# Optimization experiments

Hardware: AMD Instinct MI355X
Metric: run time of the kernel (lower is better)

Reference implementation:

```python
import jax, jax.numpy as jnp
import numpy as np

N_NODES = 100000
N_EDGES = 1000000
IN_FEAT = 128
OUT_FEAT = 128
NUM_RELS = 64
NUM_BASES = 16
SUBMAT_IN = IN_FEAT // NUM_BASES   # 8
SUBMAT_OUT = OUT_FEAT // NUM_BASES # 8


def setup_inputs() -> dict:
    key = jax.random.key(0)
    k = jax.random.split(key, 8)
    h = jax.random.normal(k[0], (N_NODES, IN_FEAT), dtype=jnp.float32)
    norm = jax.random.uniform(k[1], (N_EDGES, 1), dtype=jnp.float32)
    src = jax.random.randint(k[2], (N_EDGES,), 0, N_NODES, dtype=jnp.int32)
    dst = jax.random.randint(k[3], (N_EDGES,), 0, N_NODES, dtype=jnp.int32)
    r = jax.random.randint(k[4], (N_EDGES,), 0, NUM_RELS, dtype=jnp.int32)
    # learned params (xavier-uniform style scale)
    wscale = np.sqrt(6.0 / (SUBMAT_IN + SUBMAT_OUT)) * np.sqrt(2.0)
    weight = jax.random.uniform(k[5], (NUM_RELS, NUM_BASES * SUBMAT_IN * SUBMAT_OUT),
                                minval=-wscale, maxval=wscale, dtype=jnp.float32)
    lscale = np.sqrt(6.0 / (IN_FEAT + OUT_FEAT)) * np.sqrt(2.0)
    loop_weight = jax.random.uniform(k[6], (IN_FEAT, OUT_FEAT),
                                     minval=-lscale, maxval=lscale, dtype=jnp.float32)
    h_bias = jnp.zeros((OUT_FEAT,), dtype=jnp.float32)
    return {"h": h, "norm": norm, "weight": weight, "loop_weight": loop_weight,
            "h_bias": h_bias, "src": src, "dst": dst, "r": r}


def reference(h, norm, weight, loop_weight, h_bias, src, dst, r):
    E = src.shape[0]
    # per-edge block-diagonal weights: (E, B, si, so)
    w = weight[r].reshape(E, NUM_BASES, SUBMAT_IN, SUBMAT_OUT)
    # src features split into blocks: (E, B, si)
    hs = h[src].reshape(E, NUM_BASES, SUBMAT_IN)
    # small bmm per block, flatten to (E, OUT_FEAT)
    msg = jnp.einsum('ebi,ebio->ebo', hs, w).reshape(E, OUT_FEAT)
    msg = msg * norm
    # scatter-sum to destination nodes
    agg = jax.ops.segment_sum(msg, dst, num_segments=N_NODES)
    # self-loop message (dropout=0.0) + bias
    out = agg + h_bias + h @ loop_weight
    return jax.nn.relu(out)
```

## Files before the change

kernel.cpp:

```cpp
#include <hip/hip_runtime.h>
#include <stdint.h>

#define N_NODES 100000
#define N_EDGES 1000000
#define IN_F 128
#define OUT_F 128
#define NUM_RELS 64
#define NB_SCAN ((N_NODES + 255) / 256)
#define N_WAVES 16384
#define GATHER_B 256

typedef _Float16 half2v __attribute__((ext_vector_type(2)));

__device__ __forceinline__ float dot2f(uint32_t hu, uint32_t wu, float acc) {
#if __has_builtin(__builtin_amdgcn_fdot2)
    return __builtin_amdgcn_fdot2(__builtin_bit_cast(half2v, hu),
                                  __builtin_bit_cast(half2v, wu), acc, false);
#else
    half2v a = __builtin_bit_cast(half2v, hu);
    half2v b = __builtin_bit_cast(half2v, wu);
    acc = fmaf((float)a.x, (float)b.x, acc);
    acc = fmaf((float)a.y, (float)b.y, acc);
    return acc;
#endif
}

__device__ __forceinline__ uint32_t pkh2(float x, float y) {
    half2v v;
    v.x = (_Float16)x;
    v.y = (_Float16)y;
    return __builtin_bit_cast(uint32_t, v);
}

__global__ __launch_bounds__(256) void gemm_selfloop(
    const float* __restrict__ h, const float* __restrict__ W,
    const float* __restrict__ bias, float* __restrict__ out, int n_nodes)
{
    const int tid = threadIdx.x;
    const int ty = tid >> 4, tx = tid & 15;
    const int node0 = blockIdx.x * 128 + ty * 8;
    const int o0 = tx * 8;

    float acc[8][8];
#pragma unroll
    for (int j = 0; j < 8; ++j)
#pragma unroll
        for (int i = 0; i < 8; ++i) acc[j][i] = 0.f;

    int nidx[8];
#pragma unroll
    for (int j = 0; j < 8; ++j) {
        int n = node0 + j;
        nidx[j] = n < n_nodes ? n : (n_nodes - 1);
    }

    for (int k = 0; k < IN_F; k += 4) {
        float hsv[8][4];
#pragma unroll
        for (int j = 0; j < 8; ++j) {
            float4 hv = *reinterpret_cast<const float4*>(h + (size_t)nidx[j] * IN_F + k);
            *reinterpret_cast<float4*>(hsv[j]) = hv;
        }
#pragma unroll
        for (int kk = 0; kk < 4; ++kk) {
            const float* wrow = W + (size_t)(k + kk) * OUT_F + o0;
            float wr[8];
            *reinterpret_cast<float4*>(wr)     = *reinterpret_cast<const float4*>(wrow);
            *reinterpret_cast<float4*>(wr + 4) = *reinterpret_cast<const float4*>(wrow + 4);
#pragma unroll
            for (int j = 0; j < 8; ++j) {
                const float hk = hsv[j][kk];
#pragma unroll
                for (int i = 0; i < 8; ++i)
                    acc[j][i] = fmaf(hk, wr[i], acc[j][i]);
            }
        }
    }

    float br[8];
    *reinterpret_cast<float4*>(br)     = *reinterpret_cast<const float4*>(bias + o0);
    *reinterpret_cast<float4*>(br + 4) = *reinterpret_cast<const float4*>(bias + o0 + 4);

#pragma unroll
    for (int j = 0; j < 8; ++j) {
        int n = node0 + j;
        if (n < n_nodes) {
            float4 v0, v1;
            v0.x = acc[j][0] + br[0]; v0.y = acc[j][1] + br[1];
            v0.z = acc[j][2] + br[2]; v0.w = acc[j][3] + br[3];
            v1.x = acc[j][4] + br[4]; v1.y = acc[j][5] + br[5];
            v1.z = acc[j][6] + br[6]; v1.w = acc[j][7] + br[7];
            float* op = out + (size_t)n * OUT_F + o0;
            *reinterpret_cast<float4*>(op)     = v0;
            *reinterpret_cast<float4*>(op + 4) = v1;
        }
    }
}

__global__ __launch_bounds__(256) void prep_hist_h16(
    const float* __restrict__ weight, uint32_t* __restrict__ wsw,
    const int* __restrict__ dst, int* __restrict__ cnt,
    const float* __restrict__ h, uint4* __restrict__ h16_4,
    int n_edges, int do_h16)
{
    int t = blockIdx.x * 256 + threadIdx.x;
    if (t < NUM_RELS * 512) {
        int r    = t >> 9;
        int p    = t & 511;
        int half = p >> 8;
        int w8   = p & 255;
        int l    = w8 >> 2;
        int ip   = w8 & 3;
        int b    = l >> 2;
        int q    = l & 3;
        int o    = 2 * q + half;
        const float* s = weight + (size_t)r * 1024 + b * 64 + (2 * ip) * 8 + o;
        half2v v;
        v.x = (_Float16)s[0];
        v.y = (_Float16)s[8];
        wsw[t] = __builtin_bit_cast(uint32_t, v);
        return;
    }
    int e = t - NUM_RELS * 512;
    if (e < n_edges) {
        atomicAdd(&cnt[dst[e]], 1);
        return;
    }
    if (!do_h16) return;
    int t2 = e - n_edges;
    if (t2 < N_NODES * IN_F / 8) {
        const float4* hp = reinterpret_cast<const float4*>(h + (size_t)t2 * 8);
        float4 a = hp[0], c = hp[1];
        uint4 r;
        r.x = pkh2(a.x, a.y);
        r.y = pkh2(a.z, a.w);
        r.z = pkh2(c.x, c.y);
        r.w = pkh2(c.z, c.w);
        h16_4[t2] = r;
    }
}

__global__ __launch_bounds__(256) void block_sums(
    const int* __restrict__ cnt, int* __restrict__ part, int n)
{
    __shared__ int sdata[256];
    int i = blockIdx.x * 256 + threadIdx.x;
    sdata[threadIdx.x] = (i < n) ? cnt[i] : 0;
    __syncthreads();
    for (int s = 128; s > 0; s >>= 1) {
        if (threadIdx.x < s) sdata[threadIdx.x] += sdata[threadIdx.x + s];
        __syncthreads();
    }
    if (threadIdx.x == 0) part[blockIdx.x] = sdata[0];
}

__global__ __launch_bounds__(256) void write_off2(
    const int* __restrict__ cnt, const int* __restrict__ part,
    int* __restrict__ off, int* __restrict__ cur, int n, int n_edges)
{
    __shared__ int sdata[256];
    __shared__ int buf[256];
    const int tid = threadIdx.x;
    const int bid = blockIdx.x;

    int psum = 0;
    for (int t = tid; t < bid; t += 256) psum += part[t];
    sdata[tid] = psum;
    __syncthreads();
    for (int s = 128; s > 0; s >>= 1) {
        if (tid < s) sdata[tid] += sdata[tid + s];
        __syncthreads();
    }
    const int blockoff = sdata[0];

    int i = bid * 256 + tid;
    int v = (i < n) ? cnt[i] : 0;
    buf[tid] = v;
    __syncthreads();
    for (int ofs = 1; ofs < 256; ofs <<= 1) {
        int t = (tid >= ofs) ? buf[tid - ofs] : 0;
        __syncthreads();
        buf[tid] += t;
        __syncthreads();
    }
    int excl = buf[tid] - v + blockoff;
    if (i < n) { off[i] = excl; cur[i] = excl; }
    if (i == n - 1) off[n] = n_edges;
}

__global__ __launch_bounds__(256) void fill_and_part(
    const int* __restrict__ src, const int* __restrict__ dst,
    const int* __restrict__ rel, const float* __restrict__ norm,
    int* __restrict__ cur, int2* __restrict__ emeta,
    const int* __restrict__ off, int* __restrict__ wstart, int n_edges)
{
    int t = blockIdx.x * 256 + threadIdx.x;
    if (t < n_edges) {
        int d = dst[t];
        int p = atomicAdd(&cur[d], 1);
        int2 m;
        m.x = src[t] | (rel[t] << 20);
        m.y = __float_as_int(norm[t]);
        emeta[p] = m;
    } else {
        int w = t - n_edges;
        if (w <= N_WAVES) {
            if (w == 0) {
                wstart[0] = 0;
            } else if (w == N_WAVES) {
                wstart[N_WAVES] = N_NODES;
            } else {
                int target = (int)(((long long)N_EDGES * w) / N_WAVES);
                int lo = 0, hi = N_NODES - 1;
                while (lo < hi) {
                    int mid = (lo + hi) >> 1;
                    if (off[mid + 1] > target) hi = mid; else lo = mid + 1;
                }
                wstart[w] = lo;
            }
        } else if (w <= N_WAVES + 3) {
            int2 z; z.x = 0; z.y = 0;
            emeta[n_edges + (w - N_WAVES - 1)] = z;
        }
    }
}

__global__ __launch_bounds__(1024, 4) void gather_nodes10(
    const uint4* __restrict__ h16_4, const uint32_t* __restrict__ wsw,
    const int* __restrict__ off, const int2* __restrict__ emeta,
    const int* __restrict__ wstart, float* __restrict__ out)
{
    __shared__ uint32_t wlds[NUM_RELS * 512];

    {
        uint4* l4 = reinterpret_cast<uint4*>(wlds);
        const uint4* g4 = reinterpret_cast<const uint4*>(wsw);
        int t = threadIdx.x;
#pragma unroll
        for (int k = 0; k < 8; ++k)
            l4[t + k * 1024] = g4[t + k * 1024];
    }
    __syncthreads();

    const int lane = threadIdx.x & 63;
    const int wid  = threadIdx.x >> 6;
    const int b = lane >> 2;
    const int q = lane & 3;
    const uint32_t lbase = (uint32_t)(lane * 4);

    for (int wv = blockIdx.x * 16 + wid; wv < N_WAVES; wv += GATHER_B * 16) {
        const int n0 = wstart[wv];
        const int n1 = wstart[wv + 1];
        if (n0 >= n1) continue;

        int j = off[n0];
        int e_next = off[n0 + 1];

        int2 m0 = emeta[j];
        int2 m1 = emeta[j + 1];
        int2 m2 = emeta[j + 2];
        uint4 hv0 = h16_4[((uint32_t)m0.x & 0xFFFFFu) * 16 + b];
        uint4 hv1 = h16_4[((uint32_t)m1.x & 0xFFFFFu) * 16 + b];

        uint32_t base0 = ((uint32_t)m0.x >> 20) * 512 + lbase;
        uint4 wa = *reinterpret_cast<const uint4*>(&wlds[base0]);
        uint4 wb = *reinterpret_cast<const uint4*>(&wlds[base0 + 256]);

        for (int d = n0; d < n1; ++d) {
            const int idx2 = (d + 2 < n1) ? d + 2 : n1;
            const int e_nn = off[idx2];
            float a0 = 0.f, a1 = 0.f;

            while (j < e_next) {
                int2 m3 = emeta[j + 3];
                uint4 hv2 = h16_4[((uint32_t)m2.x & 0xFFFFFu) * 16 + b];
                uint32_t bn = ((uint32_t)m1.x >> 20) * 512 + lbase;
                uint4 wna = *reinterpret_cast<const uint4*>(&wlds[bn]);
                uint4 wnb = *reinterpret_cast<const uint4*>(&wlds[bn + 256]);

                float s0 = dot2f(hv0.x, wa.x, 0.f);
                s0 = dot2f(hv0.y, wa.y, s0);
                s0 = dot2f(hv0.z, wa.z, s0);
                s0 = dot2f(hv0.w, wa.w, s0);
                float s1 = dot2f(hv0.x, wb.x, 0.f);
                s1 = dot2f(hv0.y, wb.y, s1);
                s1 = dot2f(hv0.z, wb.z, s1);
                s1 = dot2f(hv0.w, wb.w, s1);

                const float nm = __int_as_float(m0.y);
                a0 = fmaf(s0, nm, a0);
                a1 = fmaf(s1, nm, a1);

                m0 = m1; m1 = m2; m2 = m3;
                hv0 = hv1; hv1 = hv2;
                wa = wna; wb = wnb;
                ++j;
            }

            float2* op = reinterpret_cast<float2*>(out + (size_t)d * OUT_F + b * 8 + 2 * q);
            float2 bse = *op;
            float2 res;
            res.x = fmaxf(bse.x + a0, 0.f);
            res.y = fmaxf(bse.y + a1, 0.f);
            *op = res;

            e_next = e_nn;
        }
    }
}

__global__ __launch_bounds__(1024, 4) void gather_nodes6(
    const float* __restrict__ h, const uint32_t* __restrict__ wsw,
    const int* __restrict__ off, const int2* __restrict__ emeta,
    const int* __restrict__ wstart, float* __restrict__ out)
{
    __shared__ uint32_t wlds[NUM_RELS * 512];
    {
        uint4* l4 = reinterpret_cast<uint4*>(wlds);
        const uint4* g4 = reinterpret_cast<const uint4*>(wsw);
        int t = threadIdx.x;
#pragma unroll
        for (int k = 0; k < 8; ++k)
            l4[t + k * 1024] = g4[t + k * 1024];
    }
    __syncthreads();

    const int lane = threadIdx.x & 63;
    const int wid  = threadIdx.x >> 6;
    const int b = lane >> 2;
    const int q = lane & 3;
    const uint32_t lbase = (uint32_t)(lane * 4);

    for (int wv = blockIdx.x * 16 + wid; wv < N_WAVES; wv += GATHER_B * 16) {
        const int n0 = wstart[wv];
        const int n1 = wstart[wv + 1];
        if (n0 >= n1) continue;

        int j = off[n0];
        int2 m0 = emeta[j];
        int2 m1 = emeta[j + 1];
        int2 m2 = emeta[j + 2];

        const float4* hr0 = reinterpret_cast<const float4*>(
            h + (size_t)((uint32_t)m0.x & 0xFFFFFu) * IN_F + b * 8);
        float4 h0A = hr0[0], h0B = hr0[1];
        const float4* hr1 = reinterpret_cast<const float4*>(
            h + (size_t)((uint32_t)m1.x & 0xFFFFFu) * IN_F + b * 8);
        float4 h1A = hr1[0], h1B = hr1[1];

        uint32_t base0 = ((uint32_t)m0.x >> 20) * 512 + lbase;
        uint4 wa = *reinterpret_cast<const uint4*>(&wlds[base0]);
        uint4 wb = *reinterpret_cast<const uint4*>(&wlds[base0 + 256]);

        for (int d = n0; d < n1; ++d) {
            const int end_d = off[d + 1];
            float a0 = 0.f, a1 = 0.f;

            while (j < end_d) {
                int2 m3 = emeta[j + 3];
                const float4* hr2 = reinterpret_cast<const float4*>(
                    h + (size_t)((uint32_t)m2.x & 0xFFFFFu) * IN_F + b * 8);
                float4 h2A = hr2[0], h2B = hr2[1];
                uint32_t bn = ((uint32_t)m1.x >> 20) * 512 + lbase;
                uint4 wna = *reinterpret_cast<const uint4*>(&wlds[bn]);
                uint4 wnb = *reinterpret_cast<const uint4*>(&wlds[bn + 256]);

                uint32_t h01 = __builtin_bit_cast(uint32_t, __builtin_amdgcn_cvt_pkrtz(h0A.x, h0A.y));
                uint32_t h23 = __builtin_bit_cast(uint32_t, __builtin_amdgcn_cvt_pkrtz(h0A.z, h0A.w));
                uint32_t h45 = __builtin_bit_cast(uint32_t, __builtin_amdgcn_cvt_pkrtz(h0B.x, h0B.y));
                uint32_t h67 = __builtin_bit_cast(uint32_t, __builtin_amdgcn_cvt_pkrtz(h0B.z, h0B.w));

                float s0 = dot2f(h01, wa.x, 0.f);
                s0 = dot2f(h23, wa.y, s0);
                s0 = dot2f(h45, wa.z, s0);
                s0 = dot2f(h67, wa.w, s0);
                float s1 = dot2f(h01, wb.x, 0.f);
                s1 = dot2f(h23, wb.y, s1);
                s1 = dot2f(h45, wb.z, s1);
                s1 = dot2f(h67, wb.w, s1);

                const float nm = __int_as_float(m0.y);
                a0 = fmaf(s0, nm, a0);
                a1 = fmaf(s1, nm, a1);

                m0 = m1; m1 = m2; m2 = m3;
                h0A = h1A; h0B = h1B; h1A = h2A; h1B = h2B;
                wa = wna; wb = wnb;
                ++j;
            }

            float2* op = reinterpret_cast<float2*>(out + (size_t)d * OUT_F + b * 8 + 2 * q);
            float2 bse = *op;
            float2 res;
            res.x = fmaxf(bse.x + a0, 0.f);
            res.y = fmaxf(bse.y + a1, 0.f);
            *op = res;
        }
    }
}

extern "C" void kernel_launch(void* const* d_in, const int* in_sizes, int n_in,
                              void* d_out, int out_size, void* d_ws, size_t ws_size,
                              hipStream_t stream)
{
    const float* h      = (const float*)d_in[0];
    const float* norm   = (const float*)d_in[1];
    const float* weight = (const float*)d_in[2];
    const float* loop_w = (const float*)d_in[3];
    const float* bias   = (const float*)d_in[4];
    const int*   src    = (const int*)d_in[5];
    const int*   dst    = (const int*)d_in[6];
    const int*   rel    = (const int*)d_in[7];
    float* out = (float*)d_out;

    char* wsb = (char*)d_ws;
    char* ws0 = wsb;
    int*  cnt    = (int*)wsb;  wsb += sizeof(int) * N_NODES;
    int*  off    = (int*)wsb;  wsb += sizeof(int) * (N_NODES + 1);
    int*  cur    = (int*)wsb;  wsb += sizeof(int) * N_NODES;
    int*  part   = (int*)wsb;  wsb += sizeof(int) * 512;
    int*  wstart = (int*)wsb;  wsb += sizeof(int) * (N_WAVES + 1);
    wsb = (char*)(((uintptr_t)wsb + 15) & ~(uintptr_t)15);
    uint32_t* wsw = (uint32_t*)wsb; wsb += sizeof(uint32_t) * NUM_RELS * 512;
    int2* emeta = (int2*)wsb;  wsb += sizeof(int2) * (N_EDGES + 3);
    wsb = (char*)(((uintptr_t)wsb + 15) & ~(uintptr_t)15);
    uint4* h16_4 = (uint4*)wsb; wsb += (size_t)N_NODES * IN_F * 2;

    const int use_h16 = (size_t)(wsb - ws0) <= ws_size;

    hipMemsetAsync(cnt, 0, sizeof(int) * N_NODES, stream);

    const int h16_threads = use_h16 ? (N_NODES * IN_F / 8) : 0;
    const int prep_blocks = (NUM_RELS * 512 + N_EDGES + h16_threads + 255) / 256;
    prep_hist_h16<<<prep_blocks, 256, 0, stream>>>(weight, wsw, dst, cnt,
                                                   h, h16_4, N_EDGES, use_h16);
    block_sums<<<NB_SCAN, 256, 0, stream>>>(cnt, part, N_NODES);
    write_off2<<<NB_SCAN, 256, 0, stream>>>(cnt, part, off, cur, N_NODES, N_EDGES);
    const int fp_grid = (N_EDGES + N_WAVES + 4 + 255) / 256;
    fill_and_part<<<fp_grid, 256, 0, stream>>>(src, dst, rel, norm, cur, emeta,
                                               off, wstart, N_EDGES);

    gemm_selfloop<<<(N_NODES + 127) / 128, 256, 0, stream>>>(h, loop_w, bias, out, N_NODES);
    if (use_h16) {
        gather_nodes10<<<GATHER_B, 1024, 0, stream>>>(h16_4, wsw, off, emeta, wstart, out);
    } else {
        gather_nodes6<<<GATHER_B, 1024, 0, stream>>>(h, wsw, off, emeta, wstart, out);
    }
}
```

Baseline: 319.7 us.

## Fuse the whole RGCN pipeline into one cooperative kernel with grid syncs

Replaces the memset plus six separate launches (weight swizzle, histogram, fp16 conversion, scan, CSR fill, self-loop GEMM and gather) with one cooperative persistent kernel of 256 blocks × 1024 threads. The stages are separated by grid.sync() calls, and the scan is redone with wave shuffles. The aim is to remove per-launch overhead and the idle gaps between the small preprocessing kernels. In exchange, the GEMM body now runs under a 1024-thread launch bound and may suffer register pressure. The non-cooperative fallback now always calls the fp16 gather, even when h16 does not fit in the workspace.

```diff
diff --git a/kernel.cpp b/kernel.cpp
--- a/kernel.cpp
+++ b/kernel.cpp
@@ -1,5 +1,8 @@
 #include <hip/hip_runtime.h>
+#include <hip/hip_cooperative_groups.h>
 #include <stdint.h>
+
+namespace cg = cooperative_groups;
 
 #define N_NODES 100000
 #define N_EDGES 1000000
@@ -9,6 +12,8 @@
 #define NB_SCAN ((N_NODES + 255) / 256)
 #define N_WAVES 16384
 #define GATHER_B 256
+#define GEMM_TILES ((N_NODES + 127) / 128)
+#define H16_ITEMS (N_NODES * IN_F / 8)
 
 typedef _Float16 half2v __attribute__((ext_vector_type(2)));
 
@@ -32,13 +37,22 @@
     return __builtin_bit_cast(uint32_t, v);
 }
 
-__global__ __launch_bounds__(256) void gemm_selfloop(
+__device__ __forceinline__ int wave_incl_scan(int v, int lane) {
+#pragma unroll
+    for (int o = 1; o < 64; o <<= 1) {
+        int t = __shfl_up(v, o);
+        if (lane >= o) v += t;
+    }
+    return v;
+}
+
+__device__ __forceinline__ void gemm_tile_body(
     const float* __restrict__ h, const float* __restrict__ W,
-    const float* __restrict__ bias, float* __restrict__ out, int n_nodes)
-{
-    const int tid = threadIdx.x;
+    const float* __restrict__ bias, float* __restrict__ out,
+    int tile, int tid)
+{
     const int ty = tid >> 4, tx = tid & 15;
-    const int node0 = blockIdx.x * 128 + ty * 8;
+    const int node0 = tile * 128 + ty * 8;
     const int o0 = tx * 8;
 
     float acc[8][8];
@@ -51,7 +65,7 @@
 #pragma unroll
     for (int j = 0; j < 8; ++j) {
         int n = node0 + j;
-        nidx[j] = n < n_nodes ? n : (n_nodes - 1);
+        nidx[j] = n < N_NODES ? n : (N_NODES - 1);
     }
 
     for (int k = 0; k < IN_F; k += 4) {
@@ -84,7 +98,7 @@
 #pragma unroll
     for (int j = 0; j < 8; ++j) {
         int n = node0 + j;
-        if (n < n_nodes) {
+        if (n < N_NODES) {
             float4 v0, v1;
             v0.x = acc[j][0] + br[0]; v0.y = acc[j][1] + br[1];
             v0.z = acc[j][2] + br[2]; v0.w = acc[j][3] + br[3];
@@ -97,6 +111,235 @@
     }
 }
 
+__device__ __forceinline__ void wsw_write_one(
+    const float* __restrict__ weight, uint32_t* __restrict__ wsw, int t)
+{
+    int r    = t >> 9;
+    int p    = t & 511;
+    int half = p >> 8;
+    int w8   = p & 255;
+    int l    = w8 >> 2;
+    int ip   = w8 & 3;
+    int b    = l >> 2;
+    int q    = l & 3;
+    int o    = 2 * q + half;
+    const float* s = weight + (size_t)r * 1024 + b * 64 + (2 * ip) * 8 + o;
+    half2v v;
+    v.x = (_Float16)s[0];
+    v.y = (_Float16)s[8];
+    wsw[t] = __builtin_bit_cast(uint32_t, v);
+}
+
+__device__ __forceinline__ void h16_write_one(
+    const float* __restrict__ h, uint4* __restrict__ h16_4, int t2)
+{
+    const float4* hp = reinterpret_cast<const float4*>(h + (size_t)t2 * 8);
+    float4 a = hp[0], c = hp[1];
+    uint4 r;
+    r.x = pkh2(a.x, a.y);
+    r.y = pkh2(a.z, a.w);
+    r.z = pkh2(c.x, c.y);
+    r.w = pkh2(c.z, c.w);
+    h16_4[t2] = r;
+}
+
+__global__ __launch_bounds__(1024, 4) void coop_all(
+    const float* __restrict__ h, const float* __restrict__ norm_,
+    const float* __restrict__ weight, const float* __restrict__ loop_w,
+    const float* __restrict__ bias, const int* __restrict__ src,
+    const int* __restrict__ dst, const int* __restrict__ rel,
+    float* __restrict__ out, int* __restrict__ cnt, int* __restrict__ off,
+    int* __restrict__ cur, int* __restrict__ part, int* __restrict__ wstart,
+    uint32_t* __restrict__ wsw, int2* __restrict__ emeta,
+    uint4* __restrict__ h16_4)
+{
+    __shared__ uint32_t wlds[NUM_RELS * 512];
+    __shared__ int wsum[16];
+
+    cg::grid_group grid = cg::this_grid();
+
+    const int tid  = threadIdx.x;
+    const int gtid = blockIdx.x * 1024 + tid;
+    const int NT   = GATHER_B * 1024;
+    const int lane = tid & 63;
+
+    for (int i = gtid; i < N_NODES; i += NT) cnt[i] = 0;
+    if (gtid < NUM_RELS * 512) wsw_write_one(weight, wsw, gtid);
+    for (int t2 = gtid; t2 < H16_ITEMS; t2 += NT) h16_write_one(h, h16_4, t2);
+    {
+        int group = gtid >> 8;
+        if (group < GEMM_TILES)
+            gemm_tile_body(h, loop_w, bias, out, group, gtid & 255);
+    }
+    grid.sync();
+
+    for (int e = gtid; e < N_EDGES; e += NT)
+        atomicAdd(&cnt[dst[e]], 1);
+    grid.sync();
+
+    {
+        int gw = gtid >> 6;
+        if (gw < NB_SCAN) {
+            int s = 0;
+#pragma unroll
+            for (int k = 0; k < 4; ++k) {
+                int idx = gw * 256 + k * 64 + lane;
+                s += (idx < N_NODES) ? cnt[idx] : 0;
+            }
+#pragma unroll
+            for (int o = 32; o > 0; o >>= 1) s += __shfl_xor(s, o);
+            if (lane == 0) part[gw] = s;
+        }
+    }
+    grid.sync();
+
+    if (blockIdx.x == 0) {
+        const int wid = tid >> 6;
+        if (tid < 512) {
+            int v = (tid < NB_SCAN) ? part[tid] : 0;
+            int incl = wave_incl_scan(v, lane);
+            if (lane == 63) wsum[wid] = incl;
+            __syncthreads();
+            if (wid == 0) {
+                int sv = (lane < 8) ? wsum[lane] : 0;
+                int si = wave_incl_scan(sv, lane);
+                if (lane < 8) wsum[lane] = si - sv;
+            }
+            __syncthreads();
+            part[tid] = incl - v + wsum[wid];
+        } else {
+            __syncthreads();
+            __syncthreads();
+        }
+    }
+    grid.sync();
+
+    {
+        int gw = gtid >> 6;
+        if (gw < NB_SCAN) {
+            int carry = part[gw];
+#pragma unroll
+            for (int k = 0; k < 4; ++k) {
+                int idx = gw * 256 + k * 64 + lane;
+                int v = (idx < N_NODES) ? cnt[idx] : 0;
+                int incl = wave_incl_scan(v, lane);
+                int o = carry + incl - v;
+                if (idx < N_NODES) { off[idx] = o; cur[idx] = o; }
+                carry += __shfl(incl, 63);
+            }
+        }
+        if (gtid == 0) off[N_NODES] = N_EDGES;
+    }
+    grid.sync();
+
+    for (int e = gtid; e < N_EDGES; e += NT) {
+        int d = dst[e];
+        int p = atomicAdd(&cur[d], 1);
+        int2 m;
+        m.x = src[e] | (rel[e] << 20);
+        m.y = __float_as_int(norm_[e]);
+        emeta[p] = m;
+    }
+    for (int w = gtid; w <= N_WAVES; w += NT) {
+        if (w == 0) {
+            wstart[0] = 0;
+        } else if (w == N_WAVES) {
+            wstart[N_WAVES] = N_NODES;
+        } else {
+            int target = (int)(((long long)N_EDGES * w) / N_WAVES);
+            int lo = 0, hi = N_NODES - 1;
+            while (lo < hi) {
+                int mid = (lo + hi) >> 1;
+                if (off[mid + 1] > target) hi = mid; else lo = mid + 1;
+            }
+            wstart[w] = lo;
+        }
+    }
+    if (gtid < 3) { int2 z; z.x = 0; z.y = 0; emeta[N_EDGES + gtid] = z; }
+    grid.sync();
+
+    {
+        uint4* l4 = reinterpret_cast<uint4*>(wlds);
+        const uint4* g4 = reinterpret_cast<const uint4*>(wsw);
+#pragma unroll
+        for (int k = 0; k < 8; ++k)
+            l4[tid + k * 1024] = g4[tid + k * 1024];
+    }
+    __syncthreads();
+
+    const int wid  = tid >> 6;
+    const int b = lane >> 2;
+    const int q = lane & 3;
+    const uint32_t lbase = (uint32_t)(lane * 4);
+
+    for (int wv = blockIdx.x * 16 + wid; wv < N_WAVES; wv += GATHER_B * 16) {
+        const int n0 = wstart[wv];
+        const int n1 = wstart[wv + 1];
+        if (n0 >= n1) continue;
+
+        int j = off[n0];
+        int e_next = off[n0 + 1];
+
+        int2 m0 = emeta[j];
+        int2 m1 = emeta[j + 1];
+        int2 m2 = emeta[j + 2];
+        uint4 hv0 = h16_4[((uint32_t)m0.x & 0xFFFFFu) * 16 + b];
+        uint4 hv1 = h16_4[((uint32_t)m1.x & 0xFFFFFu) * 16 + b];
+
+        uint32_t base0 = ((uint32_t)m0.x >> 20) * 512 + lbase;
+        uint4 wa = *reinterpret_cast<const uint4*>(&wlds[base0]);
+        uint4 wb = *reinterpret_cast<const uint4*>(&wlds[base0 + 256]);
+
+        for (int d = n0; d < n1; ++d) {
+            const int idx2 = (d + 2 < n1) ? d + 2 : n1;
+            const int e_nn = off[idx2];
+            float a0 = 0.f, a1 = 0.f;
+
+            while (j < e_next) {
+                int2 m3 = emeta[j + 3];
+                uint4 hv2 = h16_4[((uint32_t)m2.x & 0xFFFFFu) * 16 + b];
+                uint32_t bn = ((uint32_t)m1.x >> 20) * 512 + lbase;
+                uint4 wna = *reinterpret_cast<const uint4*>(&wlds[bn]);
+                uint4 wnb = *reinterpret_cast<const uint4*>(&wlds[bn + 256]);
+
+                float s0 = dot2f(hv0.x, wa.x, 0.f);
+                s0 = dot2f(hv0.y, wa.y, s0);
+                s0 = dot2f(hv0.z, wa.z, s0);
+                s0 = dot2f(hv0.w, wa.w, s0);
+                float s1 = dot2f(hv0.x, wb.x, 0.f);
+                s1 = dot2f(hv0.y, wb.y, s1);
+                s1 = dot2f(hv0.z, wb.z, s1);
+                s1 = dot2f(hv0.w, wb.w, s1);
+
+                const float nm = __int_as_float(m0.y);
+                a0 = fmaf(s0, nm, a0);
+                a1 = fmaf(s1, nm, a1);
+
+                m0 = m1; m1 = m2; m2 = m3;
+                hv0 = hv1; hv1 = hv2;
+                wa = wna; wb = wnb;
+                ++j;
+            }
+
+            float2* op = reinterpret_cast<float2*>(out + (size_t)d * OUT_F + b * 8 + 2 * q);
+            float2 bse = *op;
+            float2 res;
+            res.x = fmaxf(bse.x + a0, 0.f);
+            res.y = fmaxf(bse.y + a1, 0.f);
+            *op = res;
+
+            e_next = e_nn;
+        }
+    }
+}
+
+__global__ __launch_bounds__(256) void gemm_selfloop(
+    const float* __restrict__ h, const float* __restrict__ W,
+    const float* __restrict__ bias, float* __restrict__ out, int n_nodes)
+{
+    gemm_tile_body(h, W, bias, out, blockIdx.x, threadIdx.x);
+}
+
 __global__ __launch_bounds__(256) void prep_hist_h16(
     const float* __restrict__ weight, uint32_t* __restrict__ wsw,
     const int* __restrict__ dst, int* __restrict__ cnt,
@@ -105,20 +348,7 @@
 {
     int t = blockIdx.x * 256 + threadIdx.x;
     if (t < NUM_RELS * 512) {
-        int r    = t >> 9;
-        int p    = t & 511;
-        int half = p >> 8;
-        int w8   = p & 255;
-        int l    = w8 >> 2;
-        int ip   = w8 & 3;
-        int b    = l >> 2;
-        int q    = l & 3;
-        int o    = 2 * q + half;
-        const float* s = weight + (size_t)r * 1024 + b * 64 + (2 * ip) * 8 + o;
-        half2v v;
-        v.x = (_Float16)s[0];
-        v.y = (_Float16)s[8];
-        wsw[t] = __builtin_bit_cast(uint32_t, v);
+        wsw_write_one(weight, wsw, t);
         return;
     }
     int e = t - NUM_RELS * 512;
@@ -128,16 +358,7 @@
     }
     if (!do_h16) return;
     int t2 = e - n_edges;
-    if (t2 < N_NODES * IN_F / 8) {
-        const float4* hp = reinterpret_cast<const float4*>(h + (size_t)t2 * 8);
-        float4 a = hp[0], c = hp[1];
-        uint4 r;
-        r.x = pkh2(a.x, a.y);
-        r.y = pkh2(a.z, a.w);
-        r.z = pkh2(c.x, c.y);
-        r.w = pkh2(c.z, c.w);
-        h16_4[t2] = r;
-    }
+    if (t2 < H16_ITEMS) h16_write_one(h, h16_4, t2);
 }
 
 __global__ __launch_bounds__(256) void block_sums(
@@ -231,7 +452,6 @@
     const int* __restrict__ wstart, float* __restrict__ out)
 {
     __shared__ uint32_t wlds[NUM_RELS * 512];
-
     {
         uint4* l4 = reinterpret_cast<uint4*>(wlds);
         const uint4* g4 = reinterpret_cast<const uint4*>(wsw);
@@ -305,96 +525,6 @@
             *op = res;
 
             e_next = e_nn;
-        }
-    }
-}
-
-__global__ __launch_bounds__(1024, 4) void gather_nodes6(
-    const float* __restrict__ h, const uint32_t* __restrict__ wsw,
-    const int* __restrict__ off, const int2* __restrict__ emeta,
-    const int* __restrict__ wstart, float* __restrict__ out)
-{
-    __shared__ uint32_t wlds[NUM_RELS * 512];
-    {
-        uint4* l4 = reinterpret_cast<uint4*>(wlds);
-        const uint4* g4 = reinterpret_cast<const uint4*>(wsw);
-        int t = threadIdx.x;
-#pragma unroll
-        for (int k = 0; k < 8; ++k)
-            l4[t + k * 1024] = g4[t + k * 1024];
-    }
-    __syncthreads();
-
-    const int lane = threadIdx.x & 63;
-    const int wid  = threadIdx.x >> 6;
-    const int b = lane >> 2;
-    const int q = lane & 3;
-    const uint32_t lbase = (uint32_t)(lane * 4);
-
-    for (int wv = blockIdx.x * 16 + wid; wv < N_WAVES; wv += GATHER_B * 16) {
-        const int n0 = wstart[wv];
-        const int n1 = wstart[wv + 1];
-        if (n0 >= n1) continue;
-
-        int j = off[n0];
-        int2 m0 = emeta[j];
-        int2 m1 = emeta[j + 1];
-        int2 m2 = emeta[j + 2];
-
-        const float4* hr0 = reinterpret_cast<const float4*>(
-            h + (size_t)((uint32_t)m0.x & 0xFFFFFu) * IN_F + b * 8);
-        float4 h0A = hr0[0], h0B = hr0[1];
-        const float4* hr1 = reinterpret_cast<const float4*>(
-            h + (size_t)((uint32_t)m1.x & 0xFFFFFu) * IN_F + b * 8);
-        float4 h1A = hr1[0], h1B = hr1[1];
-
-        uint32_t base0 = ((uint32_t)m0.x >> 20) * 512 + lbase;
-        uint4 wa = *reinterpret_cast<const uint4*>(&wlds[base0]);
-        uint4 wb = *reinterpret_cast<const uint4*>(&wlds[base0 + 256]);
-
-        for (int d = n0; d < n1; ++d) {
-            const int end_d = off[d + 1];
-            float a0 = 0.f, a1 = 0.f;
-
-            while (j < end_d) {
-                int2 m3 = emeta[j + 3];
-                const float4* hr2 = reinterpret_cast<const float4*>(
-                    h + (size_t)((uint32_t)m2.x & 0xFFFFFu) * IN_F + b * 8);
-                float4 h2A = hr2[0], h2B = hr2[1];
-                uint32_t bn = ((uint32_t)m1.x >> 20) * 512 + lbase;
-                uint4 wna = *reinterpret_cast<const uint4*>(&wlds[bn]);
-                uint4 wnb = *reinterpret_cast<const uint4*>(&wlds[bn + 256]);
-
-                uint32_t h01 = __builtin_bit_cast(uint32_t, __builtin_amdgcn_cvt_pkrtz(h0A.x, h0A.y));
-                uint32_t h23 = __builtin_bit_cast(uint32_t, __builtin_amdgcn_cvt_pkrtz(h0A.z, h0A.w));
-                uint32_t h45 = __builtin_bit_cast(uint32_t, __builtin_amdgcn_cvt_pkrtz(h0B.x, h0B.y));
-                uint32_t h67 = __builtin_bit_cast(uint32_t, __builtin_amdgcn_cvt_pkrtz(h0B.z, h0B.w));
-
-                float s0 = dot2f(h01, wa.x, 0.f);
-                s0 = dot2f(h23, wa.y, s0);
-                s0 = dot2f(h45, wa.z, s0);
-                s0 = dot2f(h67, wa.w, s0);
-                float s1 = dot2f(h01, wb.x, 0.f);
-                s1 = dot2f(h23, wb.y, s1);
-                s1 = dot2f(h45, wb.z, s1);
-                s1 = dot2f(h67, wb.w, s1);
-
-                const float nm = __int_as_float(m0.y);
-                a0 = fmaf(s0, nm, a0);
-                a1 = fmaf(s1, nm, a1);
-
-                m0 = m1; m1 = m2; m2 = m3;
-                h0A = h1A; h0B = h1B; h1A = h2A; h1B = h2B;
-                wa = wna; wb = wnb;
-                ++j;
-            }
-
-            float2* op = reinterpret_cast<float2*>(out + (size_t)d * OUT_F + b * 8 + 2 * q);
-            float2 bse = *op;
-            float2 res;
-            res.x = fmaxf(bse.x + a0, 0.f);
-            res.y = fmaxf(bse.y + a1, 0.f);
-            *op = res;
         }
     }
 }
@@ -428,9 +558,22 @@
 
     const int use_h16 = (size_t)(wsb - ws0) <= ws_size;
 
+    if (use_h16) {
+        void* args[] = {
+            (void*)&h, (void*)&norm, (void*)&weight, (void*)&loop_w,
+            (void*)&bias, (void*)&src, (void*)&dst, (void*)&rel,
+            (void*)&out, (void*)&cnt, (void*)&off, (void*)&cur,
+            (void*)&part, (void*)&wstart, (void*)&wsw, (void*)&emeta,
+            (void*)&h16_4
+        };
+        hipError_t err = hipLaunchCooperativeKernel(
+            (const void*)coop_all, dim3(GATHER_B), dim3(1024), args, 0, stream);
+        if (err == hipSuccess) return;
+        (void)hipGetLastError();
+    }
+
     hipMemsetAsync(cnt, 0, sizeof(int) * N_NODES, stream);
-
-    const int h16_threads = use_h16 ? (N_NODES * IN_F / 8) : 0;
+    const int h16_threads = use_h16 ? H16_ITEMS : 0;
     const int prep_blocks = (NUM_RELS * 512 + N_EDGES + h16_threads + 255) / 256;
     prep_hist_h16<<<prep_blocks, 256, 0, stream>>>(weight, wsw, dst, cnt,
                                                    h, h16_4, N_EDGES, use_h16);
@@ -439,11 +582,6 @@
     const int fp_grid = (N_EDGES + N_WAVES + 4 + 255) / 256;
     fill_and_part<<<fp_grid, 256, 0, stream>>>(src, dst, rel, norm, cur, emeta,
                                                off, wstart, N_EDGES);
-
     gemm_selfloop<<<(N_NODES + 127) / 128, 256, 0, stream>>>(h, loop_w, bias, out, N_NODES);
-    if (use_h16) {
-        gather_nodes10<<<GATHER_B, 1024, 0, stream>>>(h16_4, wsw, off, emeta, wstart, out);
-    } else {
-        gather_nodes6<<<GATHER_B, 1024, 0, stream>>>(h, wsw, off, emeta, wstart, out);
-    }
-}
+    gather_nodes10<<<GATHER_B, 1024, 0, stream>>>(h16_4, wsw, off, emeta, wstart, out);
+}
```

After: 548.3 us. 71.5% more time.
